# Performance work log

Hardware: AMD Instinct MI355X
Metric: run time of the kernel (lower is better)

Reference implementation:

```python
import jax, jax.numpy as jnp
import numpy as np

N, E, D, H = 50000, 800000, 64, 4  # nodes, edges, dim_embedding (=per-head channels), heads
NEG_SLOPE = 0.2
EPS = 1e-16


def _gat(x, src, dst, W, att_src, att_dst, bias, n):
    # x: [N, Din], W: [Din, H*D] -> per-head features [N, H, D]
    xw = (x @ W).reshape(n, H, D)
    a_src = jnp.einsum('nhc,hc->nh', xw, att_src)  # [N, H]
    a_dst = jnp.einsum('nhc,hc->nh', xw, att_dst)
    logits = jax.nn.leaky_relu(a_src[src] + a_dst[dst], NEG_SLOPE)  # [E, H]
    # segment softmax over incoming edges of each destination node
    m = jax.ops.segment_max(logits, dst, num_segments=n)  # [N, H]
    ex = jnp.exp(logits - m[dst])
    s = jax.ops.segment_sum(ex, dst, num_segments=n)
    alpha = ex / (s[dst] + EPS)  # [E, H]
    msg = xw[src] * alpha[..., None]  # [E, H, D]
    out = jax.ops.segment_sum(msg, dst, num_segments=n)  # [N, H, D]
    return out.mean(axis=1) + bias  # concat=False head-mean, [N, D]


def setup_inputs() -> dict:
    key = jax.random.key(0)
    ks = jax.random.split(key, 16)
    sc = 1.0 / np.sqrt(D)
    inp = {
        'x': jax.random.normal(ks[0], (N, D), jnp.float32),
        'edge_index': jax.random.randint(ks[1], (2, E), 0, N, jnp.int64),
    }
    for i, tag in ((2, '1'), (9, '2')):
        inp['W' + tag] = jax.random.normal(ks[i], (D, H * D), jnp.float32) * sc
        inp['att_src' + tag] = jax.random.normal(ks[i + 1], (H, D), jnp.float32) * sc
        inp['att_dst' + tag] = jax.random.normal(ks[i + 2], (H, D), jnp.float32) * sc
        inp['b' + tag] = jnp.zeros((D,), jnp.float32)
        inp['lW' + tag] = jax.random.normal(ks[i + 3], (D, D), jnp.float32) * sc
        inp['lb' + tag] = jnp.zeros((D,), jnp.float32)
    return inp


def reference(x, edge_index, W1, att_src1, att_dst1, b1, lW1, lb1,
              W2, att_src2, att_dst2, b2, lW2, lb2):
    src, dst = edge_index[0], edge_index[1]
    n = x.shape[0]
    h = _gat(x, src, dst, W1, att_src1, att_dst1, b1, n) + (x @ lW1 + lb1)
    h = jax.nn.relu(h)
    out = _gat(h, src, dst, W2, att_src2, att_dst2, b2, n) + (h @ lW2 + lb2)
    return out
```

## Files before the change

### kernel.cpp

```cpp
#include <hip/hip_runtime.h>
#include <math.h>

typedef __attribute__((ext_vector_type(8))) short short8;
typedef __attribute__((ext_vector_type(4))) float f32x4;

#define NBSH 9
#define MAXBIN 128

__device__ inline unsigned fenc(float f){
  unsigned u = __float_as_uint(f);
  return u ^ ((u >> 31) ? 0xFFFFFFFFu : 0x80000000u);
}
__device__ inline float fdec(unsigned k){
  unsigned u = (k & 0x80000000u) ? (k ^ 0x80000000u) : ~k;
  return __uint_as_float(u);
}
__device__ inline unsigned short bf16rne(float f){
  unsigned u = __float_as_uint(f);
  return (unsigned short)((u + 0x7FFFu + ((u >> 16) & 1u)) >> 16);
}

__global__ __launch_bounds__(256) void k_hist(const int* __restrict__ dst, int* __restrict__ deg, int E){
  int e = blockIdx.x*256 + threadIdx.x;
  if (e < E) atomicAdd(&deg[dst[e]], 1);
}

__global__ __launch_bounds__(256) void k_scan_local(const int* __restrict__ deg, int* __restrict__ offs,
    int* __restrict__ blksum, int nelem, int ndeg){
  __shared__ int sh[256];
  int t = threadIdx.x;
  int i = blockIdx.x*256 + t;
  int v = (i < ndeg) ? deg[i] : 0;
  sh[t] = v; __syncthreads();
  for (int d = 1; d < 256; d <<= 1){
    int add = (t >= d) ? sh[t-d] : 0; __syncthreads();
    sh[t] += add; __syncthreads();
  }
  if (i < nelem) offs[i] = sh[t] - v;
  if (t == 255) blksum[blockIdx.x] = sh[t];
}

__global__ __launch_bounds__(256) void k_scan_blk(int* __restrict__ blksum, int nb){
  __shared__ int sh[256];
  int t = threadIdx.x;
  int running = 0;
  for (int base = 0; base < nb; base += 256){
    int v = (base+t < nb) ? blksum[base+t] : 0;
    __syncthreads();
    sh[t] = v; __syncthreads();
    for (int d = 1; d < 256; d <<= 1){
      int add = (t >= d) ? sh[t-d] : 0; __syncthreads();
      sh[t] += add; __syncthreads();
    }
    if (base+t < nb) blksum[base+t] = running + sh[t] - v;
    running += sh[255];
  }
}

__global__ __launch_bounds__(256) void k_scan_add(int* __restrict__ offs, const int* __restrict__ blksum,
    int* __restrict__ bincur, int nelem, int n){
  int i = blockIdx.x*256 + threadIdx.x;
  if (i < nelem){
    int v = offs[i] + blksum[blockIdx.x];
    offs[i] = v;
    if (i < n && (i & ((1<<NBSH)-1)) == 0) bincur[i >> NBSH] = v;
  }
}

__global__ __launch_bounds__(512) void k_prep(
    const float* __restrict__ W1, const float* __restrict__ as1, const float* __restrict__ ad1,
    const float* __restrict__ b1, const float* __restrict__ lb1, const float* __restrict__ lW1,
    const float* __restrict__ W2, const float* __restrict__ as2, const float* __restrict__ ad2,
    const float* __restrict__ b2, const float* __restrict__ lb2, const float* __restrict__ lW2,
    short* __restrict__ wbigT, short* __restrict__ wattBsw, float* __restrict__ bcomb,
    unsigned* __restrict__ gmax, int4* __restrict__ rec2, int* __restrict__ deg, int E, int n){
  int L = blockIdx.x;
  const float* W   = L ? W2  : W1;
  const float* asv = L ? as2 : as1;
  const float* adv = L ? ad2 : ad1;
  const float* b   = L ? b2  : b1;
  const float* lb  = L ? lb2 : lb1;
  const float* lW  = L ? lW2 : lW1;
  short* wbT = wbigT  + (size_t)L*64*328;
  short* wsw = wattBsw + L*1024;
  float* bc  = bcomb  + L*64;
  __shared__ float watt[512];
  int t = threadIdx.x;
  { int j = t >> 6, k = t & 63, h = j & 3;
    const float* att = (j < 4) ? asv : adv;
    float s = 0.f;
    for (int c = 0; c < 64; ++c) s += W[k*256 + h*64 + c] * att[h*64 + c];
    watt[j*64 + k] = s; }
  if (t < 8) gmax[t] = 0u;
  if (t < 64) bc[t] = b[t] + lb[t];
  if (L == 0 && t < 16){ int4 z; z.x = 0; z.y = 0; z.z = 0; z.w = 0; rec2[E + t] = z; }
  for (int i = L*512 + t; i < n; i += 1024) deg[i] = 0;
  __syncthreads();
  for (int i = t; i < 1024; i += 512){
    int step = i >> 9, lane = (i >> 3) & 63, j = i & 7;
    int col = lane & 15, q = lane >> 4, k = step*32 + q*8 + j;
    float v = (col < 8) ? watt[col*64 + k] : 0.f;
    wsw[i] = (short)bf16rne(v);
  }
  for (int i = t; i < 64*328; i += 512){
    int c = i / 328, q = i - c*328;
    float val = 0.f;
    if (q < 256){ int hh = q >> 6, cin = q & 63; val = 0.25f * W[cin*256 + hh*64 + c]; }
    else if (q < 320){ int kk = q - 256; val = lW[kk*64 + c]; }
    wbT[i] = (short)bf16rne(val);
  }
}

__global__ __launch_bounds__(256) void k_att(const float* __restrict__ featF,
    const unsigned short* __restrict__ featB, const short* __restrict__ wattBsw,
    float* __restrict__ asrc, float* __restrict__ adst, unsigned short* __restrict__ xbf,
    unsigned* __restrict__ gmax, int n){
  __shared__ unsigned shm[4];
  int t = threadIdx.x;
  if (t < 4) shm[t] = 0u;
  __syncthreads();
  int lane = t & 63, w = t >> 6;
  int nodebase = blockIdx.x*64 + w*16;
  int row16 = lane & 15, q = lane >> 4;
  int rowc = nodebase + row16; if (rowc > n-1) rowc = n-1;
  short8 a0, a1;
  if (featF){
    const float* fp = featF + (size_t)rowc*64;
    float4 c00 = *(const float4*)(fp + q*8);
    float4 c01 = *(const float4*)(fp + q*8 + 4);
    float4 c10 = *(const float4*)(fp + 32 + q*8);
    float4 c11 = *(const float4*)(fp + 32 + q*8 + 4);
    a0[0]=(short)bf16rne(c00.x); a0[1]=(short)bf16rne(c00.y); a0[2]=(short)bf16rne(c00.z); a0[3]=(short)bf16rne(c00.w);
    a0[4]=(short)bf16rne(c01.x); a0[5]=(short)bf16rne(c01.y); a0[6]=(short)bf16rne(c01.z); a0[7]=(short)bf16rne(c01.w);
    a1[0]=(short)bf16rne(c10.x); a1[1]=(short)bf16rne(c10.y); a1[2]=(short)bf16rne(c10.z); a1[3]=(short)bf16rne(c10.w);
    a1[4]=(short)bf16rne(c11.x); a1[5]=(short)bf16rne(c11.y); a1[6]=(short)bf16rne(c11.z); a1[7]=(short)bf16rne(c11.w);
    *(short8*)(xbf + (size_t)rowc*64 + q*8) = a0;
    *(short8*)(xbf + (size_t)rowc*64 + 32 + q*8) = a1;
  } else {
    a0 = *(const short8*)(featB + (size_t)rowc*64 + q*8);
    a1 = *(const short8*)(featB + (size_t)rowc*64 + 32 + q*8);
  }
  short8 b0 = *(const short8*)(wattBsw + lane*8);
  short8 b1 = *(const short8*)(wattBsw + 512 + lane*8);
  f32x4 acc = {0.f,0.f,0.f,0.f};
  acc = __builtin_amdgcn_mfma_f32_16x16x32_bf16(a0, b0, acc, 0, 0, 0);
  acc = __builtin_amdgcn_mfma_f32_16x16x32_bf16(a1, b1, acc, 0, 0, 0);
  int c = lane & 15;
  int rbase = nodebase + q*4;
  if (c < 8){
    float* dstp = (c < 4) ? asrc : adst;
    int hh = c & 3;
    float vmax = -INFINITY;
    #pragma unroll
    for (int r = 0; r < 4; ++r){
      int rr = rbase + r; if (rr > n-1) rr = n-1;
      dstp[(size_t)rr*4 + hh] = acc[r];
      vmax = fmaxf(vmax, acc[r]);
    }
    if (c < 4) atomicMax(&shm[hh], fenc(vmax));
  }
  __syncthreads();
  if (t < 4) atomicMax(gmax + t, shm[t]);
}

__global__ __launch_bounds__(256) void k_scatbin(const int* __restrict__ src, const int* __restrict__ dst,
    const float* __restrict__ asrc, const float* __restrict__ adst,
    int* __restrict__ bincur, const unsigned* __restrict__ gmax,
    int4* __restrict__ rec1, int E){
  __shared__ int hcnt[MAXBIN];
  __shared__ int hbase[MAXBIN];
  int t = threadIdx.x;
  int base = blockIdx.x * 4096 + t;
  if (t < MAXBIN) hcnt[t] = 0;
  __syncthreads();
  int rank[16];
  #pragma unroll
  for (int k = 0; k < 16; ++k){
    int e = base + k*256;
    rank[k] = 0;
    if (e < E){
      int d = dst[e];
      rank[k] = atomicAdd(&hcnt[d >> NBSH], 1);
    }
  }
  __syncthreads();
  if (t < MAXBIN && hcnt[t] > 0) hbase[t] = atomicAdd(&bincur[t], hcnt[t]);
  __syncthreads();
  float gm0 = fdec(gmax[0]), gm1 = fdec(gmax[1]), gm2 = fdec(gmax[2]), gm3 = fdec(gmax[3]);
  #pragma unroll
  for (int k = 0; k < 16; ++k){
    int e = base + k*256;
    if (e < E){
      int d = dst[e], s = src[e];
      float4 as = *(const float4*)(asrc + (size_t)s*4);
      float4 ad = *(const float4*)(adst + (size_t)d*4);
      float g0 = gm0 + ad.x; g0 = fmaxf(g0, 0.2f*g0);
      float g1 = gm1 + ad.y; g1 = fmaxf(g1, 0.2f*g1);
      float g2 = gm2 + ad.z; g2 = fmaxf(g2, 0.2f*g2);
      float g3 = gm3 + ad.w; g3 = fmaxf(g3, 0.2f*g3);
      float l0 = as.x + ad.x; l0 = fmaxf(l0, 0.2f*l0);
      float l1 = as.y + ad.y; l1 = fmaxf(l1, 0.2f*l1);
      float l2 = as.z + ad.z; l2 = fmaxf(l2, 0.2f*l2);
      float l3 = as.w + ad.w; l3 = fmaxf(l3, 0.2f*l3);
      unsigned lo = (unsigned)bf16rne(__expf(l0 - g0)) | ((unsigned)bf16rne(__expf(l1 - g1)) << 16);
      unsigned hi = (unsigned)bf16rne(__expf(l2 - g2)) | ((unsigned)bf16rne(__expf(l3 - g3)) << 16);
      int4 rv; rv.x = (int)lo; rv.y = (int)hi; rv.z = s; rv.w = d;
      rec1[hbase[d >> NBSH] + rank[k]] = rv;
    }
  }
}

__global__ __launch_bounds__(256) void k_place(const int4* __restrict__ rec1,
    const int* __restrict__ offs, int4* __restrict__ rec2, int n){
  __shared__ int cur[1 << NBSH];
  int t = threadIdx.x;
  int nodebase = blockIdx.x << NBSH;
  int nodeend = nodebase + (1 << NBSH); if (nodeend > n) nodeend = n;
  for (int i = t; i < (1 << NBSH); i += 256) cur[i] = 0;
  __syncthreads();
  int winlo = offs[nodebase], winhi = offs[nodeend];
  for (int i = winlo + t; i < winhi; i += 256){
    int4 r = rec1[i];
    int d = r.w;
    int pos = offs[d] + atomicAdd(&cur[d - nodebase], 1);
    rec2[pos] = r;
  }
}

__global__ __launch_bounds__(256) void k_edge2(int4* __restrict__ rec,
    const float* __restrict__ asrc, const float* __restrict__ adst,
    const unsigned* __restrict__ gmax, int E){
  int i = blockIdx.x*256 + threadIdx.x;
  if (i >= E) return;
  int4 r = rec[i];
  int s = r.z, d = r.w;
  float4 as = *(const float4*)(asrc + (size_t)s*4);
  float4 ad = *(const float4*)(adst + (size_t)d*4);
  float g0 = fdec(gmax[0]) + ad.x; g0 = fmaxf(g0, 0.2f*g0);
  float g1 = fdec(gmax[1]) + ad.y; g1 = fmaxf(g1, 0.2f*g1);
  float g2 = fdec(gmax[2]) + ad.z; g2 = fmaxf(g2, 0.2f*g2);
  float g3 = fdec(gmax[3]) + ad.w; g3 = fmaxf(g3, 0.2f*g3);
  float l0 = as.x + ad.x; l0 = fmaxf(l0, 0.2f*l0);
  float l1 = as.y + ad.y; l1 = fmaxf(l1, 0.2f*l1);
  float l2 = as.z + ad.z; l2 = fmaxf(l2, 0.2f*l2);
  float l3 = as.w + ad.w; l3 = fmaxf(l3, 0.2f*l3);
  r.x = (int)((unsigned)bf16rne(__expf(l0 - g0)) | ((unsigned)bf16rne(__expf(l1 - g1)) << 16));
  r.y = (int)((unsigned)bf16rne(__expf(l2 - g2)) | ((unsigned)bf16rne(__expf(l3 - g3)) << 16));
  rec[i] = r;
}

__global__ __launch_bounds__(256) void k_agg(const int4* __restrict__ rec,
    const int* __restrict__ offs, const unsigned short* __restrict__ xbf,
    short* __restrict__ Abf, int n){
  int wid = threadIdx.x >> 6;
  int lane = threadIdx.x & 63;
  int v = blockIdx.x*4 + wid;
  if (v >= n) return;
  int rs = __builtin_amdgcn_readfirstlane(offs[v]);
  int re = __builtin_amdgcn_readfirstlane(offs[v+1]);
  int nrem = re - rs;
  const int4* rp = rec + rs;
  float s0=0.f,s1=0.f,s2=0.f,s3=0.f;
  float a0=0.f,a1=0.f,a2=0.f,a3=0.f;

#define ACC(LO,HI,XU) { \
    float xc = __uint_as_float(((unsigned)(XU)) << 16); \
    float p0 = __uint_as_float((LO) << 16); \
    float p1 = __uint_as_float((LO) & 0xFFFF0000u); \
    float p2 = __uint_as_float((HI) << 16); \
    float p3 = __uint_as_float((HI) & 0xFFFF0000u); \
    s0 += p0; s1 += p1; s2 += p2; s3 += p3; \
    a0 = fmaf(p0, xc, a0); a1 = fmaf(p1, xc, a1); \
    a2 = fmaf(p2, xc, a2); a3 = fmaf(p3, xc, a3); }

  int nch = nrem >> 2;
  if (nch > 0){
    int4 R0[4], R1[4], T[4], U[4];
    unsigned xw0[4], xw1[4];
    #pragma unroll
    for (int j = 0; j < 4; ++j) R0[j] = rp[j];
    #pragma unroll
    for (int j = 0; j < 4; ++j) xw0[j] = xbf[(((size_t)(unsigned)R0[j].z)<<6)+lane];
    #pragma unroll
    for (int j = 0; j < 4; ++j) R1[j] = rp[4+j];
    int c = 0;
    for (; c + 1 < nch; c += 2){
      #pragma unroll
      for (int j = 0; j < 4; ++j) T[j] = rp[((c+2)<<2)+j];
      #pragma unroll
      for (int j = 0; j < 4; ++j) xw1[j] = xbf[(((size_t)(unsigned)R1[j].z)<<6)+lane];
      #pragma unroll
      for (int j = 0; j < 4; ++j) U[j] = rp[((c+3)<<2)+j];
      #pragma unroll
      for (int j = 0; j < 4; ++j) ACC((unsigned)R0[j].x, (unsigned)R0[j].y, xw0[j]);
      #pragma unroll
      for (int j = 0; j < 4; ++j) R0[j] = T[j];
      #pragma unroll
      for (int j = 0; j < 4; ++j) xw0[j] = xbf[(((size_t)(unsigned)R0[j].z)<<6)+lane];
      #pragma unroll
      for (int j = 0; j < 4; ++j) ACC((unsigned)R1[j].x, (unsigned)R1[j].y, xw1[j]);
      #pragma unroll
      for (int j = 0; j < 4; ++j) R1[j] = U[j];
    }
    if (c < nch){
      #pragma unroll
      for (int j = 0; j < 4; ++j) ACC((unsigned)R0[j].x, (unsigned)R0[j].y, xw0[j]);
    }
  }
  for (int i = nch<<2; i < nrem; ++i){
    int4 t = rp[i];
    unsigned xt = xbf[(((size_t)(unsigned)t.z)<<6)+lane];
    ACC((unsigned)t.x, (unsigned)t.y, xt);
  }
#undef ACC
  size_t base = (size_t)v*256 + lane;
  Abf[base +   0] = (short)bf16rne(a0 / (s0 + 1e-16f));
  Abf[base +  64] = (short)bf16rne(a1 / (s1 + 1e-16f));
  Abf[base + 128] = (short)bf16rne(a2 / (s2 + 1e-16f));
  Abf[base + 192] = (short)bf16rne(a3 / (s3 + 1e-16f));
}

__global__ __launch_bounds__(256) void k_out(const short* __restrict__ Abf,
    const unsigned short* __restrict__ xbf, const short* __restrict__ wbigT,
    const float* __restrict__ bcomb, float* __restrict__ outF, unsigned short* __restrict__ outB, int n){
  __shared__ __align__(16) short sB[64*328];
  {
    const short8* gs = (const short8*)wbigT;
    short8* ls = (short8*)sB;
    for (int i = threadIdx.x; i < 64*328/8; i += 256) ls[i] = gs[i];
  }
  __syncthreads();
  int lane = threadIdx.x & 63, wid = threadIdx.x >> 6;
  int rowbase = blockIdx.x*64 + wid*16;
  int arow = rowbase + (lane & 15); if (arow > n-1) arow = n-1;
  int ksub = (lane >> 4) * 8;
  const short* ap = Abf + (size_t)arow*256 + ksub;
  const short* xp = (const short*)xbf + (size_t)arow*64 + ksub;
  const short* bp = sB + (lane & 15)*328 + ksub;
  f32x4 acc0 = {0.f,0.f,0.f,0.f}, acc1 = acc0, acc2 = acc0, acc3 = acc0;
  #pragma unroll
  for (int k0 = 0; k0 < 320; k0 += 32){
    short8 a  = (k0 < 256) ? *(const short8*)(ap + k0) : *(const short8*)(xp + (k0 - 256));
    short8 b0 = *(const short8*)(bp + k0);
    short8 b1 = *(const short8*)(bp + 16*328 + k0);
    short8 b2 = *(const short8*)(bp + 32*328 + k0);
    short8 b3 = *(const short8*)(bp + 48*328 + k0);
    acc0 = __builtin_amdgcn_mfma_f32_16x16x32_bf16(a, b0, acc0, 0, 0, 0);
    acc1 = __builtin_amdgcn_mfma_f32_16x16x32_bf16(a, b1, acc1, 0, 0, 0);
    acc2 = __builtin_amdgcn_mfma_f32_16x16x32_bf16(a, b2, acc2, 0, 0, 0);
    acc3 = __builtin_amdgcn_mfma_f32_16x16x32_bf16(a, b3, acc3, 0, 0, 0);
  }
  int ccol = lane & 15;
  int crow = rowbase + (lane >> 4)*4;
  float bb0 = bcomb[ 0 + ccol];
  float bb1 = bcomb[16 + ccol];
  float bb2 = bcomb[32 + ccol];
  float bb3 = bcomb[48 + ccol];
  #pragma unroll
  for (int r = 0; r < 4; ++r){
    int rr = crow + r;
    if (rr < n){
      float o0 = acc0[r] + bb0, o1 = acc1[r] + bb1, o2 = acc2[r] + bb2, o3 = acc3[r] + bb3;
      if (outB){
        unsigned short* orow = outB + (size_t)rr*64;
        orow[ 0 + ccol] = bf16rne(fmaxf(o0, 0.f));
        orow[16 + ccol] = bf16rne(fmaxf(o1, 0.f));
        orow[32 + ccol] = bf16rne(fmaxf(o2, 0.f));
        orow[48 + ccol] = bf16rne(fmaxf(o3, 0.f));
      } else {
        float* orow = outF + (size_t)rr*64;
        orow[ 0 + ccol] = o0;
        orow[16 + ccol] = o1;
        orow[32 + ccol] = o2;
        orow[48 + ccol] = o3;
      }
    }
  }
}

extern "C" void kernel_launch(void* const* d_in, const int* in_sizes, int n_in,
                              void* d_out, int out_size, void* d_ws, size_t ws_size,
                              hipStream_t stream){
  const float* x   = (const float*)d_in[0];
  const int*   ei  = (const int*)d_in[1];
  const float* W1  = (const float*)d_in[2];
  const float* as1 = (const float*)d_in[3];
  const float* ad1 = (const float*)d_in[4];
  const float* b1  = (const float*)d_in[5];
  const float* lW1 = (const float*)d_in[6];
  const float* lb1 = (const float*)d_in[7];
  const float* W2  = (const float*)d_in[8];
  const float* as2 = (const float*)d_in[9];
  const float* ad2 = (const float*)d_in[10];
  const float* b2  = (const float*)d_in[11];
  const float* lW2 = (const float*)d_in[12];
  const float* lb2 = (const float*)d_in[13];
  int N = in_sizes[0] / 64;
  int E = in_sizes[1] / 2;
  const int* srce = ei;
  const int* dste = ei + E;

  char* w = (char*)d_ws;
  size_t off = 0;
  auto alloc = [&](size_t bytes)->char*{
    char* p = w + off; off = (off + bytes + 255) & ~(size_t)255; return p;
  };
  int*      offs    = (int*)     alloc((size_t)(N+1)*4);
  int*      deg     = (int*)     alloc((size_t)N*4);
  int*      bincur  = (int*)     alloc(MAXBIN*4);
  int*      blksum  = (int*)     alloc(4096);
  int4*     rec1    = (int4*)    alloc((size_t)E*16);
  int4*     rec2    = (int4*)    alloc((size_t)(E+16)*16);
  short*    wbigT   = (short*)   alloc((size_t)2*64*328*2);
  short*    wattBsw = (short*)   alloc(2*1024*2);
  float*    bcomb   = (float*)   alloc(2*64*4);
  unsigned* gmax    = (unsigned*)alloc(32);
  float*    pasrc   = (float*)   alloc((size_t)N*16);
  float*    padst   = (float*)   alloc((size_t)N*16);
  short*    Abf     = (short*)   alloc((size_t)N*256*2);
  unsigned short* xbf1 = (unsigned short*)alloc((size_t)N*64*2);
  unsigned short* xbf2 = (unsigned short*)alloc((size_t)N*64*2);
  (void)ws_size; (void)n_in; (void)out_size;

  int gE = (E + 255)/256;
  int nelem = N + 1;
  int nb = (nelem + 255)/256;
  int gATT = (N + 63)/64;
  int gOUT = (N + 63)/64;
  int gSB  = (E + 4095)/4096;
  int nbin = (N + (1<<NBSH) - 1) >> NBSH;
  int gAGG = (N + 3)/4;
  float* outp = (float*)d_out;

  k_prep<<<2, 512, 0, stream>>>(W1, as1, ad1, b1, lb1, lW1,
                                W2, as2, ad2, b2, lb2, lW2,
                                wbigT, wattBsw, bcomb, gmax, rec2, deg, E, N);

  k_hist<<<gE, 256, 0, stream>>>(dste, deg, E);
  k_scan_local<<<nb, 256, 0, stream>>>(deg, offs, blksum, nelem, N);
  k_scan_blk<<<1, 256, 0, stream>>>(blksum, nb);
  k_scan_add<<<nb, 256, 0, stream>>>(offs, blksum, bincur, nelem, N);

  k_att <<<gATT, 256, 0, stream>>>(x, nullptr, wattBsw, pasrc, padst, xbf1, gmax, N);
  k_scatbin<<<gSB, 256, 0, stream>>>(srce, dste, pasrc, padst, bincur, gmax, rec1, E);
  k_place<<<nbin, 256, 0, stream>>>(rec1, offs, rec2, N);
  k_agg <<<gAGG, 256, 0, stream>>>(rec2, offs, xbf1, Abf, N);
  k_out <<<gOUT, 256, 0, stream>>>(Abf, xbf1, wbigT, bcomb, nullptr, xbf2, N);

  k_att <<<gATT, 256, 0, stream>>>(nullptr, xbf2, wattBsw + 1024, pasrc, padst, nullptr, gmax + 4, N);
  k_edge2<<<gE, 256, 0, stream>>>(rec2, pasrc, padst, gmax + 4, E);
  k_agg <<<gAGG, 256, 0, stream>>>(rec2, offs, xbf2, Abf, N);
  k_out <<<gOUT, 256, 0, stream>>>(Abf, xbf2, wbigT + 64*328, bcomb + 64, outp, nullptr, N);
}
```

Measured before the change: 233.8 us.

## Fuse three-kernel prefix scan into one decoupled scan; read k_out weights from global

Replaces the local-scan, block-scan and add kernels with a single kernel. Each block publishes its partial sum with a flag, then waits on the flags of all earlier blocks and sums their partials, which removes two kernel launches. Separately, k_out no longer stages the 42 KB weight matrix into LDS and reads B fragments directly from global memory through the cache. The spin-wait assumes all earlier blocks become resident, which holds for about 196 blocks but would deadlock if the block count exceeded 256. Dropping the LDS stage frees shared memory and raises occupancy, at the cost of more global and cache traffic per MFMA.

```diff
diff --git a/kernel.cpp b/kernel.cpp
--- a/kernel.cpp
+++ b/kernel.cpp
@@ -25,45 +25,41 @@
   if (e < E) atomicAdd(&deg[dst[e]], 1);
 }
 
-__global__ __launch_bounds__(256) void k_scan_local(const int* __restrict__ deg, int* __restrict__ offs,
-    int* __restrict__ blksum, int nelem, int ndeg){
+__global__ __launch_bounds__(256) void k_scan(const int* __restrict__ deg, int* __restrict__ offs,
+    int* __restrict__ partials, int* __restrict__ flags, int* __restrict__ bincur,
+    int nelem, int ndeg){
   __shared__ int sh[256];
-  int t = threadIdx.x;
-  int i = blockIdx.x*256 + t;
+  __shared__ int sh2[256];
+  int t = threadIdx.x, b = blockIdx.x;
+  int i = b*256 + t;
   int v = (i < ndeg) ? deg[i] : 0;
   sh[t] = v; __syncthreads();
   for (int d = 1; d < 256; d <<= 1){
     int add = (t >= d) ? sh[t-d] : 0; __syncthreads();
     sh[t] += add; __syncthreads();
   }
-  if (i < nelem) offs[i] = sh[t] - v;
-  if (t == 255) blksum[blockIdx.x] = sh[t];
-}
-
-__global__ __launch_bounds__(256) void k_scan_blk(int* __restrict__ blksum, int nb){
-  __shared__ int sh[256];
-  int t = threadIdx.x;
-  int running = 0;
-  for (int base = 0; base < nb; base += 256){
-    int v = (base+t < nb) ? blksum[base+t] : 0;
+  if (t == 255){
+    partials[b] = sh[255];
+    __threadfence();
+    atomicExch(&flags[b], 1);
+  }
+  int myp = 0;
+  if (t < b){
+    while (atomicAdd(&flags[t], 0) == 0){}
+    myp = atomicAdd(&partials[t], 0);
+  }
+  __syncthreads();
+  sh2[t] = myp; __syncthreads();
+  #pragma unroll
+  for (int d = 128; d >= 1; d >>= 1){
+    if (t < d) sh2[t] += sh2[t + d];
     __syncthreads();
-    sh[t] = v; __syncthreads();
-    for (int d = 1; d < 256; d <<= 1){
-      int add = (t >= d) ? sh[t-d] : 0; __syncthreads();
-      sh[t] += add; __syncthreads();
-    }
-    if (base+t < nb) blksum[base+t] = running + sh[t] - v;
-    running += sh[255];
-  }
-}
-
-__global__ __launch_bounds__(256) void k_scan_add(int* __restrict__ offs, const int* __restrict__ blksum,
-    int* __restrict__ bincur, int nelem, int n){
-  int i = blockIdx.x*256 + threadIdx.x;
+  }
+  int off = sh2[0];
   if (i < nelem){
-    int v = offs[i] + blksum[blockIdx.x];
-    offs[i] = v;
-    if (i < n && (i & ((1<<NBSH)-1)) == 0) bincur[i >> NBSH] = v;
+    int val = off + sh[t] - v;
+    offs[i] = val;
+    if (i < ndeg && (i & ((1<<NBSH)-1)) == 0) bincur[i >> NBSH] = val;
   }
 }
 
@@ -73,7 +69,8 @@
     const float* __restrict__ W2, const float* __restrict__ as2, const float* __restrict__ ad2,
     const float* __restrict__ b2, const float* __restrict__ lb2, const float* __restrict__ lW2,
     short* __restrict__ wbigT, short* __restrict__ wattBsw, float* __restrict__ bcomb,
-    unsigned* __restrict__ gmax, int4* __restrict__ rec2, int* __restrict__ deg, int E, int n){
+    unsigned* __restrict__ gmax, int4* __restrict__ rec2, int* __restrict__ deg,
+    int* __restrict__ flags, int E, int n){
   int L = blockIdx.x;
   const float* W   = L ? W2  : W1;
   const float* asv = L ? as2 : as1;
@@ -94,6 +91,7 @@
   if (t < 8) gmax[t] = 0u;
   if (t < 64) bc[t] = b[t] + lb[t];
   if (L == 0 && t < 16){ int4 z; z.x = 0; z.y = 0; z.z = 0; z.w = 0; rec2[E + t] = z; }
+  if (L == 1 && t < 256) flags[t] = 0;
   for (int i = L*512 + t; i < n; i += 1024) deg[i] = 0;
   __syncthreads();
   for (int i = t; i < 1024; i += 512){
@@ -323,20 +321,13 @@
 __global__ __launch_bounds__(256) void k_out(const short* __restrict__ Abf,
     const unsigned short* __restrict__ xbf, const short* __restrict__ wbigT,
     const float* __restrict__ bcomb, float* __restrict__ outF, unsigned short* __restrict__ outB, int n){
-  __shared__ __align__(16) short sB[64*328];
-  {
-    const short8* gs = (const short8*)wbigT;
-    short8* ls = (short8*)sB;
-    for (int i = threadIdx.x; i < 64*328/8; i += 256) ls[i] = gs[i];
-  }
-  __syncthreads();
   int lane = threadIdx.x & 63, wid = threadIdx.x >> 6;
   int rowbase = blockIdx.x*64 + wid*16;
   int arow = rowbase + (lane & 15); if (arow > n-1) arow = n-1;
   int ksub = (lane >> 4) * 8;
   const short* ap = Abf + (size_t)arow*256 + ksub;
   const short* xp = (const short*)xbf + (size_t)arow*64 + ksub;
-  const short* bp = sB + (lane & 15)*328 + ksub;
+  const short* bp = wbigT + (lane & 15)*328 + ksub;
   f32x4 acc0 = {0.f,0.f,0.f,0.f}, acc1 = acc0, acc2 = acc0, acc3 = acc0;
   #pragma unroll
   for (int k0 = 0; k0 < 320; k0 += 32){
@@ -408,7 +399,8 @@
   int*      offs    = (int*)     alloc((size_t)(N+1)*4);
   int*      deg     = (int*)     alloc((size_t)N*4);
   int*      bincur  = (int*)     alloc(MAXBIN*4);
-  int*      blksum  = (int*)     alloc(4096);
+  int*      partials= (int*)     alloc(256*4);
+  int*      flags   = (int*)     alloc(256*4);
   int4*     rec1    = (int4*)    alloc((size_t)E*16);
   int4*     rec2    = (int4*)    alloc((size_t)(E+16)*16);
   short*    wbigT   = (short*)   alloc((size_t)2*64*328*2);
@@ -434,12 +426,10 @@
 
   k_prep<<<2, 512, 0, stream>>>(W1, as1, ad1, b1, lb1, lW1,
                                 W2, as2, ad2, b2, lb2, lW2,
-                                wbigT, wattBsw, bcomb, gmax, rec2, deg, E, N);
+                                wbigT, wattBsw, bcomb, gmax, rec2, deg, flags, E, N);
 
   k_hist<<<gE, 256, 0, stream>>>(dste, deg, E);
-  k_scan_local<<<nb, 256, 0, stream>>>(deg, offs, blksum, nelem, N);
-  k_scan_blk<<<1, 256, 0, stream>>>(blksum, nb);
-  k_scan_add<<<nb, 256, 0, stream>>>(offs, blksum, bincur, nelem, N);
+  k_scan<<<nb, 256, 0, stream>>>(deg, offs, partials, flags, bincur, nelem, N);
 
   k_att <<<gATT, 256, 0, stream>>>(x, nullptr, wattBsw, pasrc, padst, xbf1, gmax, N);
   k_scatbin<<<gSB, 256, 0, stream>>>(srce, dste, pasrc, padst, bincur, gmax, rec1, E);
```

Result: no change. 236.4 us (+1.1%).
